# Kernel optimization log

Measured on AMD Instinct MI355X. Metric: run time of the kernel, lower is better.

## Reference

```python
import jax, jax.numpy as jnp
import numpy as np

N_NODES = 100_000
E_TOTAL = 1_100_000
# up_scale_edge_ranges: static metadata on the Data object -> baked as constants
EXCLUDE_RANGES = [(1_000_000, 1_100_000)]
_mask = np.ones(E_TOTAL, dtype=bool)
for _s, _e in EXCLUDE_RANGES:
    _mask[_s:_e] = False
KEEP_IDX = np.nonzero(_mask)[0]  # static, shape [1_000_000]


def _mlp(h, w1, b1, w2, b2):
    return jax.nn.relu(h @ w1 + b1) @ w2 + b2


def setup_inputs() -> dict:
    key = jax.random.key(0)
    ks = jax.random.split(key, 12)
    s = 0.05
    return {
        "x": jax.random.normal(ks[0], (N_NODES, 7), dtype=jnp.float32),
        "pos": jax.random.normal(ks[1], (N_NODES, 3), dtype=jnp.float32),
        "edge_index": jax.random.randint(ks[2], (2, E_TOTAL), 0, N_NODES, dtype=jnp.int64),
        "nw1": jax.random.normal(ks[3], (7, 128), dtype=jnp.float32) * s,
        "nb1": jnp.zeros((128,), dtype=jnp.float32),
        "nw2": jax.random.normal(ks[4], (128, 128), dtype=jnp.float32) * s,
        "nb2": jnp.zeros((128,), dtype=jnp.float32),
        "ew1": jax.random.normal(ks[5], (3, 128), dtype=jnp.float32) * s,
        "eb1": jnp.zeros((128,), dtype=jnp.float32),
        "ew2": jax.random.normal(ks[6], (128, 128), dtype=jnp.float32) * s,
        "eb2": jnp.zeros((128,), dtype=jnp.float32),
    }


def reference(x, pos, edge_index, nw1, nb1, nw2, nb2, ew1, eb1, ew2, eb2):
    # static mask over edge ranges (shapes fixed at trace time)
    edges = edge_index[:, KEEP_IDX]                       # [2, E_kept]
    d = pos[edges[0], :2] - pos[edges[1], :2]             # [E_kept, 2]
    norm = jnp.linalg.norm(d, axis=1, keepdims=True)      # [E_kept, 1]
    edges_attr = jnp.concatenate([d, norm], axis=1)       # [E_kept, 3]
    edge_embedding = _mlp(edges_attr, ew1, eb1, ew2, eb2) # [E_kept, 128]
    node_embedding = _mlp(x, nw1, nb1, nw2, nb2)          # [N, 128]
    return (node_embedding, edge_embedding)
```

## Files before the change

kernel.cpp:

```cpp
#include <hip/hip_runtime.h>

typedef short short8 __attribute__((ext_vector_type(8)));
typedef float f32x4 __attribute__((ext_vector_type(4)));

#define N_NODES   100000
#define E_KEEP    1000000
#define E_TOTAL_N 1100000
#define EDGE_OUT_BASE 12800000L

__device__ __forceinline__ unsigned short f2bf(float f) {
  unsigned int u = __builtin_bit_cast(unsigned int, f);
  u += 0x7fffu + ((u >> 16) & 1u);
  return (unsigned short)(u >> 16);
}

__global__ void transpose_w2(const float* __restrict__ nw2,
                             const float* __restrict__ ew2,
                             unsigned short* __restrict__ ws) {
  int idx = blockIdx.x * 256 + threadIdx.x;
  for (int i = idx; i < 32768; i += 8192) {
    int m = i >> 14;
    int w = i & 16383;
    int k = w >> 7;
    int n = w & 127;
    const float* src = m ? ew2 : nw2;
    ws[m * 16384 + n * 128 + k] = f2bf(src[w]);
  }
}

__device__ __forceinline__ void run_edges(
    const float* __restrict__ pos,
    const int* __restrict__ ei,
    const float* __restrict__ w1,
    const float* __restrict__ b1,
    const float* __restrict__ b2,
    const unsigned short* __restrict__ w2t,
    float* __restrict__ outp,
    int bid)
{
  __shared__ float w1f[3 * 128];
  __shared__ float b1f[128];
  __shared__ float b2f[128];
  int t = threadIdx.x;
  if (t < 128) { b1f[t] = b1[t]; b2f[t] = b2[t]; }
  for (int i = t; i < 384; i += 256) w1f[i] = w1[i];
  __syncthreads();

  const int lane = t & 63;
  const int wid  = t >> 6;
  const int rg   = wid & 1;
  const int wc   = wid >> 1;
  const int c    = lane & 15;
  const int g    = lane >> 4;

  short8 wfrag[4][4];
#pragma unroll
  for (int nf = 0; nf < 4; ++nf)
#pragma unroll
    for (int kk = 0; kk < 4; ++kk)
      wfrag[nf][kk] = *(const short8*)(w2t + (wc * 64 + nf * 16 + c) * 128 + kk * 32 + g * 8);

  int srcs[8], dsts[8];
#pragma unroll
  for (int s = 0; s < 8; ++s) {
    int r  = bid * 256 + s * 32 + rg * 16 + c;
    int rl = r < E_KEEP ? r : E_KEEP - 1;
    srcs[s] = ei[rl];
    dsts[s] = ei[E_TOTAL_N + rl];
  }
  float pxa[8], pya[8], pxb[8], pyb[8];
#pragma unroll
  for (int s = 0; s < 8; ++s) {
    pxa[s] = pos[srcs[s] * 3];
    pya[s] = pos[srcs[s] * 3 + 1];
    pxb[s] = pos[dsts[s] * 3];
    pyb[s] = pos[dsts[s] * 3 + 1];
  }

#pragma unroll
  for (int s = 0; s < 8; ++s) {
    int row0 = bid * 256 + s * 32 + rg * 16;
    if (row0 >= E_KEEP) continue;

    float ax = pxa[s] - pxb[s];
    float ay = pya[s] - pyb[s];
    float an = sqrtf(ax * ax + ay * ay);

    short8 hfrag[4];
#pragma unroll
    for (int kk = 0; kk < 4; ++kk) {
      int k0 = kk * 32 + g * 8;
      const f32x4* bp  = (const f32x4*)&b1f[k0];
      f32x4 h0 = bp[0], h1 = bp[1];
      const f32x4* w0p = (const f32x4*)&w1f[k0];
      const f32x4* w1p = (const f32x4*)&w1f[128 + k0];
      const f32x4* w2p = (const f32x4*)&w1f[256 + k0];
      h0 += ax * w0p[0]; h1 += ax * w0p[1];
      h0 += ay * w1p[0]; h1 += ay * w1p[1];
      h0 += an * w2p[0]; h1 += an * w2p[1];
      short8 hf;
#pragma unroll
      for (int j = 0; j < 4; ++j) hf[j]     = (short)f2bf(fmaxf(h0[j], 0.f));
#pragma unroll
      for (int j = 0; j < 4; ++j) hf[4 + j] = (short)f2bf(fmaxf(h1[j], 0.f));
      hfrag[kk] = hf;
    }

    f32x4 acc[4] = {};
#pragma unroll
    for (int kk = 0; kk < 4; ++kk)
#pragma unroll
      for (int nf = 0; nf < 4; ++nf)
        acc[nf] = __builtin_amdgcn_mfma_f32_16x16x32_bf16(wfrag[nf][kk], hfrag[kk], acc[nf], 0, 0, 0);

    int r = row0 + c;
    if (r < E_KEEP) {
      long base = EDGE_OUT_BASE + (long)r * 128;
#pragma unroll
      for (int nf = 0; nf < 4; ++nf) {
        int col0 = wc * 64 + nf * 16 + g * 4;
        f32x4 bv = *(const f32x4*)&b2f[col0];
        f32x4 o = acc[nf] + bv;
        *(f32x4*)(outp + base + col0) = o;
      }
    }
  }
}

__device__ __forceinline__ void run_nodes(
    const float* __restrict__ xin,
    const float* __restrict__ w1,
    const float* __restrict__ b1,
    const float* __restrict__ b2,
    const unsigned short* __restrict__ w2t,
    float* __restrict__ outp,
    int bid)
{
  __shared__ float w1fn[7 * 128];
  __shared__ float b1fn[128];
  __shared__ float b2fn[128];
  int t = threadIdx.x;
  if (t < 128) { b1fn[t] = b1[t]; b2fn[t] = b2[t]; }
  for (int i = t; i < 896; i += 256) w1fn[i] = w1[i];
  __syncthreads();

  const int lane = t & 63;
  const int wid  = t >> 6;
  const int rg   = wid & 1;
  const int wc   = wid >> 1;
  const int c    = lane & 15;
  const int g    = lane >> 4;

  short8 wfrag[4][4];
#pragma unroll
  for (int nf = 0; nf < 4; ++nf)
#pragma unroll
    for (int kk = 0; kk < 4; ++kk)
      wfrag[nf][kk] = *(const short8*)(w2t + (wc * 64 + nf * 16 + c) * 128 + kk * 32 + g * 8);

#pragma unroll
  for (int s = 0; s < 8; ++s) {
    int row0 = bid * 256 + s * 32 + rg * 16;
    if (row0 >= N_NODES) continue;
    int r  = row0 + c;
    int rl = r < N_NODES ? r : N_NODES - 1;

    float a[7];
#pragma unroll
    for (int cc = 0; cc < 7; ++cc) a[cc] = xin[rl * 7 + cc];

    short8 hfrag[4];
#pragma unroll
    for (int kk = 0; kk < 4; ++kk) {
      int k0 = kk * 32 + g * 8;
      const f32x4* bp = (const f32x4*)&b1fn[k0];
      f32x4 h0 = bp[0], h1 = bp[1];
#pragma unroll
      for (int cc = 0; cc < 7; ++cc) {
        const f32x4* wp = (const f32x4*)&w1fn[cc * 128 + k0];
        h0 += a[cc] * wp[0];
        h1 += a[cc] * wp[1];
      }
      short8 hf;
#pragma unroll
      for (int j = 0; j < 4; ++j) hf[j]     = (short)f2bf(fmaxf(h0[j], 0.f));
#pragma unroll
      for (int j = 0; j < 4; ++j) hf[4 + j] = (short)f2bf(fmaxf(h1[j], 0.f));
      hfrag[kk] = hf;
    }

    f32x4 acc[4] = {};
#pragma unroll
    for (int kk = 0; kk < 4; ++kk)
#pragma unroll
      for (int nf = 0; nf < 4; ++nf)
        acc[nf] = __builtin_amdgcn_mfma_f32_16x16x32_bf16(wfrag[nf][kk], hfrag[kk], acc[nf], 0, 0, 0);

    if (r < N_NODES) {
      long base = (long)r * 128;
#pragma unroll
      for (int nf = 0; nf < 4; ++nf) {
        int col0 = wc * 64 + nf * 16 + g * 4;
        f32x4 bv = *(const f32x4*)&b2fn[col0];
        f32x4 o = acc[nf] + bv;
        *(f32x4*)(outp + base + col0) = o;
      }
    }
  }
}

__global__ __launch_bounds__(256, 2) void encoder_kernel(
    const float* __restrict__ x,
    const float* __restrict__ pos,
    const int* __restrict__ ei,
    const float* __restrict__ nw1,
    const float* __restrict__ nb1,
    const float* __restrict__ nb2,
    const float* __restrict__ ew1,
    const float* __restrict__ eb1,
    const float* __restrict__ eb2,
    const unsigned short* __restrict__ ws,
    float* __restrict__ outp,
    int nodeBlocks)
{
  int bid = blockIdx.x;
  if (bid < nodeBlocks) {
    run_nodes(x, nw1, nb1, nb2, ws, outp, bid);
  } else {
    run_edges(pos, ei, ew1, eb1, eb2, ws + 16384, outp, bid - nodeBlocks);
  }
}

extern "C" void kernel_launch(void* const* d_in, const int* in_sizes, int n_in,
                              void* d_out, int out_size, void* d_ws, size_t ws_size,
                              hipStream_t stream) {
  const float* x   = (const float*)d_in[0];
  const float* pos = (const float*)d_in[1];
  const int*   ei  = (const int*)d_in[2];
  const float* nw1 = (const float*)d_in[3];
  const float* nb1 = (const float*)d_in[4];
  const float* nw2 = (const float*)d_in[5];
  const float* nb2 = (const float*)d_in[6];
  const float* ew1 = (const float*)d_in[7];
  const float* eb1 = (const float*)d_in[8];
  const float* ew2 = (const float*)d_in[9];
  const float* eb2 = (const float*)d_in[10];
  unsigned short* ws   = (unsigned short*)d_ws;
  float*          outp = (float*)d_out;

  transpose_w2<<<32, 256, 0, stream>>>(nw2, ew2, ws);

  int nodeBlocks = (N_NODES + 255) / 256;
  int edgeBlocks = (E_KEEP + 255) / 256;
  encoder_kernel<<<nodeBlocks + edgeBlocks, 256, 0, stream>>>(
      x, pos, ei, nw1, nb1, nb2, ew1, eb1, eb2, ws, outp, nodeBlocks);
}
```

Measured before the change: 193.3 us.

## Split output columns across eight waves per block to raise occupancy

Blocks grow from 256 to 512 threads, and each wave now computes 32 output columns instead of 64. That halves the per-wave B-fragment registers and accumulators, and the launch bounds rise to 4 blocks per CU. The edge path drops its upfront prefetch of all eight edges' indices and positions and gathers them per iteration instead, interleaving the layer-1 compute with the MFMAs. The aim is more resident waves to hide gather and store latency, at the cost of less per-wave instruction-level parallelism on the gathers.

```diff
diff --git a/kernel.cpp b/kernel.cpp
--- a/kernel.cpp
+++ b/kernel.cpp
@@ -12,6 +12,15 @@
   unsigned int u = __builtin_bit_cast(unsigned int, f);
   u += 0x7fffu + ((u >> 16) & 1u);
   return (unsigned short)(u >> 16);
+}
+
+__device__ __forceinline__ short8 mk_hfrag(f32x4 h0, f32x4 h1) {
+  short8 hf;
+#pragma unroll
+  for (int j = 0; j < 4; ++j) hf[j]     = (short)f2bf(fmaxf(h0[j], 0.f));
+#pragma unroll
+  for (int j = 0; j < 4; ++j) hf[4 + j] = (short)f2bf(fmaxf(h1[j], 0.f));
+  return hf;
 }
 
 __global__ void transpose_w2(const float* __restrict__ nw2,
@@ -27,6 +36,7 @@
     ws[m * 16384 + n * 128 + k] = f2bf(src[w]);
   }
 }
+
 
 __device__ __forceinline__ void run_edges(
     const float* __restrict__ pos,
@@ -43,7 +53,7 @@
   __shared__ float b2f[128];
   int t = threadIdx.x;
   if (t < 128) { b1f[t] = b1[t]; b2f[t] = b2[t]; }
-  for (int i = t; i < 384; i += 256) w1f[i] = w1[i];
+  else if (t < 512) w1f[t - 128] = w1[t - 128];
   __syncthreads();
 
   const int lane = t & 63;
@@ -53,76 +63,46 @@
   const int c    = lane & 15;
   const int g    = lane >> 4;
 
-  short8 wfrag[4][4];
-#pragma unroll
-  for (int nf = 0; nf < 4; ++nf)
+  short8 wfrag[2][4];
+#pragma unroll
+  for (int nf = 0; nf < 2; ++nf)
 #pragma unroll
     for (int kk = 0; kk < 4; ++kk)
-      wfrag[nf][kk] = *(const short8*)(w2t + (wc * 64 + nf * 16 + c) * 128 + kk * 32 + g * 8);
-
-  int srcs[8], dsts[8];
-#pragma unroll
+      wfrag[nf][kk] = *(const short8*)(w2t + (wc * 32 + nf * 16 + c) * 128 + kk * 32 + g * 8);
+
+  f32x4 b2v0 = *(const f32x4*)&b2f[wc * 32 + g * 4];
+  f32x4 b2v1 = *(const f32x4*)&b2f[wc * 32 + 16 + g * 4];
+
   for (int s = 0; s < 8; ++s) {
     int r  = bid * 256 + s * 32 + rg * 16 + c;
     int rl = r < E_KEEP ? r : E_KEEP - 1;
-    srcs[s] = ei[rl];
-    dsts[s] = ei[E_TOTAL_N + rl];
-  }
-  float pxa[8], pya[8], pxb[8], pyb[8];
-#pragma unroll
-  for (int s = 0; s < 8; ++s) {
-    pxa[s] = pos[srcs[s] * 3];
-    pya[s] = pos[srcs[s] * 3 + 1];
-    pxb[s] = pos[dsts[s] * 3];
-    pyb[s] = pos[dsts[s] * 3 + 1];
-  }
-
-#pragma unroll
-  for (int s = 0; s < 8; ++s) {
-    int row0 = bid * 256 + s * 32 + rg * 16;
-    if (row0 >= E_KEEP) continue;
-
-    float ax = pxa[s] - pxb[s];
-    float ay = pya[s] - pyb[s];
+    int si = ei[rl];
+    int di = ei[E_TOTAL_N + rl];
+    float ax = pos[si * 3]     - pos[di * 3];
+    float ay = pos[si * 3 + 1] - pos[di * 3 + 1];
     float an = sqrtf(ax * ax + ay * ay);
 
-    short8 hfrag[4];
+    f32x4 a0 = {}, a1 = {};
 #pragma unroll
     for (int kk = 0; kk < 4; ++kk) {
       int k0 = kk * 32 + g * 8;
-      const f32x4* bp  = (const f32x4*)&b1f[k0];
-      f32x4 h0 = bp[0], h1 = bp[1];
-      const f32x4* w0p = (const f32x4*)&w1f[k0];
-      const f32x4* w1p = (const f32x4*)&w1f[128 + k0];
-      const f32x4* w2p = (const f32x4*)&w1f[256 + k0];
-      h0 += ax * w0p[0]; h1 += ax * w0p[1];
-      h0 += ay * w1p[0]; h1 += ay * w1p[1];
-      h0 += an * w2p[0]; h1 += an * w2p[1];
-      short8 hf;
-#pragma unroll
-      for (int j = 0; j < 4; ++j) hf[j]     = (short)f2bf(fmaxf(h0[j], 0.f));
-#pragma unroll
-      for (int j = 0; j < 4; ++j) hf[4 + j] = (short)f2bf(fmaxf(h1[j], 0.f));
-      hfrag[kk] = hf;
-    }
-
-    f32x4 acc[4] = {};
-#pragma unroll
-    for (int kk = 0; kk < 4; ++kk)
-#pragma unroll
-      for (int nf = 0; nf < 4; ++nf)
-        acc[nf] = __builtin_amdgcn_mfma_f32_16x16x32_bf16(wfrag[nf][kk], hfrag[kk], acc[nf], 0, 0, 0);
-
-    int r = row0 + c;
+      f32x4 h0 = *(const f32x4*)&b1f[k0];
+      f32x4 h1 = *(const f32x4*)&b1f[k0 + 4];
+      h0 += ax * *(const f32x4*)&w1f[k0];
+      h1 += ax * *(const f32x4*)&w1f[k0 + 4];
+      h0 += ay * *(const f32x4*)&w1f[128 + k0];
+      h1 += ay * *(const f32x4*)&w1f[128 + k0 + 4];
+      h0 += an * *(const f32x4*)&w1f[256 + k0];
+      h1 += an * *(const f32x4*)&w1f[256 + k0 + 4];
+      short8 hf = mk_hfrag(h0, h1);
+      a0 = __builtin_amdgcn_mfma_f32_16x16x32_bf16(wfrag[0][kk], hf, a0, 0, 0, 0);
+      a1 = __builtin_amdgcn_mfma_f32_16x16x32_bf16(wfrag[1][kk], hf, a1, 0, 0, 0);
+    }
+
     if (r < E_KEEP) {
-      long base = EDGE_OUT_BASE + (long)r * 128;
-#pragma unroll
-      for (int nf = 0; nf < 4; ++nf) {
-        int col0 = wc * 64 + nf * 16 + g * 4;
-        f32x4 bv = *(const f32x4*)&b2f[col0];
-        f32x4 o = acc[nf] + bv;
-        *(f32x4*)(outp + base + col0) = o;
-      }
+      float* base = outp + EDGE_OUT_BASE + (long)r * 128 + wc * 32 + g * 4;
+      *(f32x4*)(base)      = a0 + b2v0;
+      *(f32x4*)(base + 16) = a1 + b2v1;
     }
   }
 }
@@ -141,7 +121,7 @@
   __shared__ float b2fn[128];
   int t = threadIdx.x;
   if (t < 128) { b1fn[t] = b1[t]; b2fn[t] = b2[t]; }
-  for (int i = t; i < 896; i += 256) w1fn[i] = w1[i];
+  for (int i = t; i < 896; i += 512) w1fn[i] = w1[i];
   __syncthreads();
 
   const int lane = t & 63;
@@ -151,14 +131,16 @@
   const int c    = lane & 15;
   const int g    = lane >> 4;
 
-  short8 wfrag[4][4];
-#pragma unroll
-  for (int nf = 0; nf < 4; ++nf)
+  short8 wfrag[2][4];
+#pragma unroll
+  for (int nf = 0; nf < 2; ++nf)
 #pragma unroll
     for (int kk = 0; kk < 4; ++kk)
-      wfrag[nf][kk] = *(const short8*)(w2t + (wc * 64 + nf * 16 + c) * 128 + kk * 32 + g * 8);
-
-#pragma unroll
+      wfrag[nf][kk] = *(const short8*)(w2t + (wc * 32 + nf * 16 + c) * 128 + kk * 32 + g * 8);
+
+  f32x4 b2v0 = *(const f32x4*)&b2fn[wc * 32 + g * 4];
+  f32x4 b2v1 = *(const f32x4*)&b2fn[wc * 32 + 16 + g * 4];
+
   for (int s = 0; s < 8; ++s) {
     int row0 = bid * 256 + s * 32 + rg * 16;
     if (row0 >= N_NODES) continue;
@@ -169,47 +151,31 @@
 #pragma unroll
     for (int cc = 0; cc < 7; ++cc) a[cc] = xin[rl * 7 + cc];
 
-    short8 hfrag[4];
+    f32x4 a0 = {}, a1 = {};
 #pragma unroll
     for (int kk = 0; kk < 4; ++kk) {
       int k0 = kk * 32 + g * 8;
-      const f32x4* bp = (const f32x4*)&b1fn[k0];
-      f32x4 h0 = bp[0], h1 = bp[1];
+      f32x4 h0 = *(const f32x4*)&b1fn[k0];
+      f32x4 h1 = *(const f32x4*)&b1fn[k0 + 4];
 #pragma unroll
       for (int cc = 0; cc < 7; ++cc) {
-        const f32x4* wp = (const f32x4*)&w1fn[cc * 128 + k0];
-        h0 += a[cc] * wp[0];
-        h1 += a[cc] * wp[1];
+        h0 += a[cc] * *(const f32x4*)&w1fn[cc * 128 + k0];
+        h1 += a[cc] * *(const f32x4*)&w1fn[cc * 128 + k0 + 4];
       }
-      short8 hf;
-#pragma unroll
-      for (int j = 0; j < 4; ++j) hf[j]     = (short)f2bf(fmaxf(h0[j], 0.f));
-#pragma unroll
-      for (int j = 0; j < 4; ++j) hf[4 + j] = (short)f2bf(fmaxf(h1[j], 0.f));
-      hfrag[kk] = hf;
-    }
-
-    f32x4 acc[4] = {};
-#pragma unroll
-    for (int kk = 0; kk < 4; ++kk)
-#pragma unroll
-      for (int nf = 0; nf < 4; ++nf)
-        acc[nf] = __builtin_amdgcn_mfma_f32_16x16x32_bf16(wfrag[nf][kk], hfrag[kk], acc[nf], 0, 0, 0);
+      short8 hf = mk_hfrag(h0, h1);
+      a0 = __builtin_amdgcn_mfma_f32_16x16x32_bf16(wfrag[0][kk], hf, a0, 0, 0, 0);
+      a1 = __builtin_amdgcn_mfma_f32_16x16x32_bf16(wfrag[1][kk], hf, a1, 0, 0, 0);
+    }
 
     if (r < N_NODES) {
-      long base = (long)r * 128;
-#pragma unroll
-      for (int nf = 0; nf < 4; ++nf) {
-        int col0 = wc * 64 + nf * 16 + g * 4;
-        f32x4 bv = *(const f32x4*)&b2fn[col0];
-        f32x4 o = acc[nf] + bv;
-        *(f32x4*)(outp + base + col0) = o;
-      }
-    }
-  }
-}
-
-__global__ __launch_bounds__(256, 2) void encoder_kernel(
+      float* base = outp + (long)r * 128 + wc * 32 + g * 4;
+      *(f32x4*)(base)      = a0 + b2v0;
+      *(f32x4*)(base + 16) = a1 + b2v1;
+    }
+  }
+}
+
+__global__ __launch_bounds__(512, 4) void encoder_kernel(
     const float* __restrict__ x,
     const float* __restrict__ pos,
     const int* __restrict__ ei,
@@ -252,6 +218,6 @@
 
   int nodeBlocks = (N_NODES + 255) / 256;
   int edgeBlocks = (E_KEEP + 255) / 256;
-  encoder_kernel<<<nodeBlocks + edgeBlocks, 256, 0, stream>>>(
+  encoder_kernel<<<nodeBlocks + edgeBlocks, 512, 0, stream>>>(
       x, pos, ei, nw1, nb1, nb2, ew1, eb1, eb2, ws, outp, nodeBlocks);
 }
```

Result: slower. 770.5 us (+298.6%).
